# Kernel optimization log

Measured on AMD Instinct MI355X. Metric: run time of the kernel, lower is better.

Reference implementation:

```python
import jax, jax.numpy as jnp
import numpy as np

D_MODEL = 1024
N_HEADS = 16
HEAD_DIM = D_MODEL // N_HEADS
D_LATENT = 256
LAMBDA_DECAY = 0.01
TIME_STEP = 0.01  # get_timestamps spacing; wall-clock base cancels in diffs
CLAMP = 1e4


def setup_inputs() -> dict:
    key = jax.random.key(0)
    ks = jax.random.split(key, 8)
    B, S = 2, 2048
    def w(k, i, o):
        return jax.random.normal(k, (i, o), dtype=jnp.float32) * 0.02
    return {
        "x": jax.random.normal(ks[0], (B, S, D_MODEL), dtype=jnp.float32),
        "Wq": w(ks[1], D_MODEL, D_MODEL),
        "Wk": w(ks[2], D_MODEL, D_MODEL),
        "Wv": w(ks[3], D_MODEL, D_MODEL),
        "Wo": w(ks[4], D_MODEL, D_MODEL),
        "W_down_kv": w(ks[5], D_MODEL, D_LATENT),
        "W_up_k": w(ks[6], D_LATENT, D_MODEL),
        "W_up_v": w(ks[7], D_LATENT, D_MODEL),
    }


def reference(x, Wq, Wk, Wv, Wo, W_down_kv, W_up_k, W_up_v):
    B, S, _ = x.shape
    q = x @ Wq
    k = x @ Wk
    v = x @ Wv
    latent_kv = (k + v) @ W_down_kv            # [B,S,d_latent]
    k_rec = latent_kv @ W_up_k                 # [B,S,d_model]
    v_rec = latent_kv @ W_up_v
    # split heads -> [B,H,S,hd]
    def heads(t):
        return t.reshape(B, S, N_HEADS, HEAD_DIM).transpose(0, 2, 1, 3)
    qh, kh, vh = heads(q), heads(k_rec), heads(v_rec)
    scale = 1.0 / (jnp.sqrt(jnp.float32(D_MODEL)) + 1e-8)
    scores = jnp.einsum("bhqd,bhkd->bhqk", qh, kh) * scale
    scores = jnp.clip(jnp.nan_to_num(scores, nan=-1e9), -CLAMP, CLAMP)
    # time decay: |t_i - t_j| = TIME_STEP * |i - j| (wall-clock base cancels)
    idx = jnp.arange(S, dtype=jnp.float32)
    decay = jnp.exp(-LAMBDA_DECAY * TIME_STEP * jnp.abs(idx[:, None] - idx[None, :]))
    scores = scores * decay[None, None, :, :]
    scores = jnp.clip(jnp.nan_to_num(scores, nan=-1e9), -CLAMP, CLAMP)
    attn = jax.nn.softmax(scores, axis=-1)
    out = jnp.einsum("bhqk,bhkd->bhqd", attn, vh)
    out = out.transpose(0, 2, 1, 3).reshape(B, S, D_MODEL)
    return out @ Wo, latent_kv
```

## Files before the change

kernel.cpp:

```cpp
#include <hip/hip_runtime.h>
#include <hip/hip_bf16.h>
#include <cstdint>
#include <cstddef>

typedef __bf16 bf16;
typedef __bf16 bf16x8 __attribute__((ext_vector_type(8)));
typedef float f32x4 __attribute__((ext_vector_type(4)));

#define NB 2
#define SEQ 2048
#define DM 1024
#define MTOK 4096
#define DL 256
#define NH 16
#define HD 64

#define LOG2E 1.4426950408889634f

__device__ __forceinline__ void gload16(const void* g, void* l) {
  __builtin_amdgcn_global_load_lds((const __attribute__((address_space(1))) void*)g,
                                   (__attribute__((address_space(3))) void*)l, 16, 0, 0);
}
__device__ __forceinline__ float fast_exp2(float x) {
#if __has_builtin(__builtin_amdgcn_exp2f)
  return __builtin_amdgcn_exp2f(x);
#else
  float r; asm("v_exp_f32 %0, %1" : "=v"(r) : "v"(x)); return r;
#endif
}
__device__ __forceinline__ int xcd_swz(int orig, int nwg) {
  int x = orig & 7;
  int q = nwg >> 3, r = nwg & 7;
  int base = (x < r) ? x * (q + 1) : r * (q + 1) + (x - r) * q;
  return base + (orig >> 3);
}

__device__ __forceinline__ void transpose_dev(const float* __restrict__ in0,
                                              bf16* __restrict__ out, int R, int C,
                                              int c0, int r0, int tid, float (*tile)[33]) {
  int tx = tid & 31, ty = tid >> 5;
#pragma unroll
  for (int i = 0; i < 4; ++i) {
    int r = r0 + ty + 8 * i;
    tile[ty + 8 * i][tx] = in0[(size_t)r * C + c0 + tx];
  }
  __syncthreads();
  int c = tid >> 3, s = tid & 7;
  bf16 o4[4] __attribute__((aligned(8)));
#pragma unroll
  for (int j = 0; j < 4; ++j) o4[j] = (bf16)tile[4 * s + j][c];
  *reinterpret_cast<uint2*>(out + (size_t)(c0 + c) * R + r0 + 4 * s) =
      *reinterpret_cast<const uint2*>(o4);
}

__device__ __forceinline__ void cvt8_dev(const float* __restrict__ in, bf16* __restrict__ out,
                                         int blk, int tid) {
  int i = (blk * 256 + tid) * 8;
  float4 a = *reinterpret_cast<const float4*>(in + i);
  float4 b = *reinterpret_cast<const float4*>(in + i + 4);
  bf16 o[8] __attribute__((aligned(16)));
  o[0] = (bf16)a.x; o[1] = (bf16)a.y; o[2] = (bf16)a.z; o[3] = (bf16)a.w;
  o[4] = (bf16)b.x; o[5] = (bf16)b.y; o[6] = (bf16)b.z; o[7] = (bf16)b.w;
  *reinterpret_cast<uint4*>(out + i) = *reinterpret_cast<const uint4*>(o);
}

__device__ __forceinline__ void sum8_dev(const float* __restrict__ in0, const float* __restrict__ in1,
                                         bf16* __restrict__ out, int blk, int tid) {
  int i = (blk * 256 + tid) * 8;
  float4 a0 = *reinterpret_cast<const float4*>(in0 + i);
  float4 b0 = *reinterpret_cast<const float4*>(in0 + i + 4);
  float4 a1 = *reinterpret_cast<const float4*>(in1 + i);
  float4 b1 = *reinterpret_cast<const float4*>(in1 + i + 4);
  bf16 o[8] __attribute__((aligned(16)));
  o[0] = (bf16)(a0.x + a1.x); o[1] = (bf16)(a0.y + a1.y);
  o[2] = (bf16)(a0.z + a1.z); o[3] = (bf16)(a0.w + a1.w);
  o[4] = (bf16)(b0.x + b1.x); o[5] = (bf16)(b0.y + b1.y);
  o[6] = (bf16)(b0.z + b1.z); o[7] = (bf16)(b0.w + b1.w);
  *reinterpret_cast<uint4*>(out + i) = *reinterpret_cast<const uint4*>(o);
}

__global__ __launch_bounds__(256) void prep_kernel(const float* __restrict__ x,
                                                   const float* __restrict__ Wq,
                                                   const float* __restrict__ Wk,
                                                   const float* __restrict__ Wv,
                                                   const float* __restrict__ Wo,
                                                   const float* __restrict__ Wdn,
                                                   const float* __restrict__ Wuk,
                                                   const float* __restrict__ Wuv,
                                                   bf16* xbf, bf16* WqT, bf16* WoT, bf16* WdnT,
                                                   bf16* WukT, bf16* WuvT, bf16* Wkv) {
  __shared__ float tile[32][33];
  int id = blockIdx.x, tid = threadIdx.x;
  if (id < 2048) { cvt8_dev(x, xbf, id, tid); return; }
  id -= 2048;
  if (id < 512) { sum8_dev(Wk, Wv, Wkv, id, tid); return; }
  id -= 512;
  if (id < 1024) { transpose_dev(Wq, WqT, 1024, 1024, (id & 31) * 32, (id >> 5) * 32, tid, tile); return; }
  id -= 1024;
  if (id < 1024) { transpose_dev(Wo, WoT, 1024, 1024, (id & 31) * 32, (id >> 5) * 32, tid, tile); return; }
  id -= 1024;
  if (id < 256) { transpose_dev(Wdn, WdnT, 1024, 256, (id & 7) * 32, (id >> 3) * 32, tid, tile); return; }
  id -= 256;
  if (id < 256) { transpose_dev(Wuk, WukT, 256, 1024, (id & 31) * 32, (id >> 5) * 32, tid, tile); return; }
  id -= 256;
  transpose_dev(Wuv, WuvT, 256, 1024, (id & 31) * 32, (id >> 5) * 32, tid, tile);
}

template <int TN, int EPI>
__device__ __forceinline__ void gemm_core(const bf16* __restrict__ A, const bf16* __restrict__ Bt,
                                          bf16* __restrict__ O1, float* __restrict__ Of,
                                          int K, int bx, int by, bf16* As, bf16* Bs) {
  const int tid = threadIdx.x;
  const int lane = tid & 63;
  const int wv = tid >> 6;
  const int wr = wv >> 1, wc = wv & 1;
  const int row0 = bx * 128, col0 = by * TN;
  const int l15 = lane & 15;
  const int kq = (lane >> 4) * 8;
  constexpr int NR = TN / 32;
  constexpr int BSZ = TN * 32;

  const bf16* aS = A + (size_t)(row0 + (tid >> 2)) * K + (tid & 3) * 8;
  const bf16* bS = Bt + (size_t)(col0 + (tid >> 2)) * K + (tid & 3) * 8;
  const int d0 = tid * 8, d1 = tid * 8 + 2048;

  gload16(aS, As + d0); gload16(aS + (size_t)64 * K, As + d1);
  gload16(bS, Bs + d0);
  if constexpr (TN == 128) gload16(bS + (size_t)64 * K, Bs + d1);
  aS += 32; bS += 32;

  f32x4 acc[4][NR] = {};
  int cur = 0;
  for (int k0 = 0; k0 < K; k0 += 32) {
    __syncthreads();
    if (k0 + 32 < K) {
      const int nxA = (cur ^ 1) * 4096, nxB = (cur ^ 1) * BSZ;
      gload16(aS, As + nxA + d0); gload16(aS + (size_t)64 * K, As + nxA + d1);
      gload16(bS, Bs + nxB + d0);
      if constexpr (TN == 128) gload16(bS + (size_t)64 * K, Bs + nxB + d1);
      aS += 32; bS += 32;
    }
    const bf16* Ab = As + cur * 4096;
    const bf16* Bb = Bs + cur * BSZ;
    bf16x8 af[4], bfr[NR];
#pragma unroll
    for (int m = 0; m < 4; ++m)
      af[m] = *reinterpret_cast<const bf16x8*>(&Ab[(wr * 64 + m * 16 + l15) * 32 + kq]);
#pragma unroll
    for (int n = 0; n < NR; ++n)
      bfr[n] = *reinterpret_cast<const bf16x8*>(&Bb[(wc * (TN / 2) + n * 16 + l15) * 32 + kq]);
    __builtin_amdgcn_s_setprio(1);
#pragma unroll
    for (int m = 0; m < 4; ++m)
#pragma unroll
      for (int n = 0; n < NR; ++n)
        acc[m][n] = __builtin_amdgcn_mfma_f32_16x16x32_bf16(af[m], bfr[n], acc[m][n], 0, 0, 0);
    __builtin_amdgcn_s_setprio(0);
    cur ^= 1;
  }

  const int rbase = row0 + wr * 64 + (lane >> 4) * 4;
  const int cbase = col0 + wc * (TN / 2) + l15;
#pragma unroll
  for (int m = 0; m < 4; ++m) {
#pragma unroll
    for (int n = 0; n < NR; ++n) {
      const int cc = cbase + n * 16;
      if constexpr (EPI == 0) {
#pragma unroll
        for (int r = 0; r < 4; ++r)
          O1[(size_t)(rbase + m * 16 + r) * DM + cc] = (bf16)acc[m][n][r];
      } else if constexpr (EPI == 3) {
#pragma unroll
        for (int r = 0; r < 4; ++r)
          Of[(size_t)(rbase + m * 16 + r) * DM + cc] = acc[m][n][r];
      } else {
#pragma unroll
        for (int r = 0; r < 4; ++r)
          O1[(size_t)(rbase + m * 16 + r) * MTOK + cc] = (bf16)acc[m][n][r];
      }
    }
  }
}

__device__ __forceinline__ void gemm64_lat(const bf16* __restrict__ A, const bf16* __restrict__ Bt,
                                           bf16* __restrict__ O1, float* __restrict__ Of,
                                           int K, int bx, int by, bf16* As, bf16* Bs) {
  const int tid = threadIdx.x;
  const int lane = tid & 63;
  const int wv = tid >> 6;
  const int wr = wv >> 1, wc = wv & 1;
  const int row0 = bx * 64, col0 = by * 64;
  const int l15 = lane & 15;
  const int kq = (lane >> 4) * 8;

  const bf16* aS = A + (size_t)(row0 + (tid >> 2)) * K + (tid & 3) * 8;
  const bf16* bS = Bt + (size_t)(col0 + (tid >> 2)) * K + (tid & 3) * 8;
  const int d0 = tid * 8;

  gload16(aS, As + d0); gload16(bS, Bs + d0);
  aS += 32; bS += 32;

  f32x4 acc[2][2] = {};
  int cur = 0;
  for (int k0 = 0; k0 < K; k0 += 32) {
    __syncthreads();
    if (k0 + 32 < K) {
      const int nx = (cur ^ 1) * 2048;
      gload16(aS, As + nx + d0); gload16(bS, Bs + nx + d0);
      aS += 32; bS += 32;
    }
    const bf16* Ab = As + cur * 2048;
    const bf16* Bb = Bs + cur * 2048;
    bf16x8 af[2], bfr[2];
#pragma unroll
    for (int m = 0; m < 2; ++m)
      af[m] = *reinterpret_cast<const bf16x8*>(&Ab[(wr * 32 + m * 16 + l15) * 32 + kq]);
#pragma unroll
    for (int n = 0; n < 2; ++n)
      bfr[n] = *reinterpret_cast<const bf16x8*>(&Bb[(wc * 32 + n * 16 + l15) * 32 + kq]);
    __builtin_amdgcn_s_setprio(1);
#pragma unroll
    for (int m = 0; m < 2; ++m)
#pragma unroll
      for (int n = 0; n < 2; ++n)
        acc[m][n] = __builtin_amdgcn_mfma_f32_16x16x32_bf16(af[m], bfr[n], acc[m][n], 0, 0, 0);
    __builtin_amdgcn_s_setprio(0);
    cur ^= 1;
  }

  const int rbase = row0 + wr * 32 + (lane >> 4) * 4;
  const int cbase = col0 + wc * 32 + l15;
#pragma unroll
  for (int m = 0; m < 2; ++m)
#pragma unroll
    for (int n = 0; n < 2; ++n)
#pragma unroll
      for (int r = 0; r < 4; ++r) {
        float v = acc[m][n][r];
        O1[(size_t)(rbase + m * 16 + r) * DL + (cbase + n * 16)] = (bf16)v;
        Of[(size_t)(rbase + m * 16 + r) * DL + (cbase + n * 16)] = v;
      }
}

__global__ __launch_bounds__(256) void gemm_q_w(const bf16* __restrict__ xbf,
                                                const bf16* __restrict__ WqT, bf16* qbf,
                                                const bf16* __restrict__ WdnT,
                                                const bf16* __restrict__ Wkv, bf16* WkvdT) {
  __shared__ __align__(16) bf16 As[2 * 4096];
  __shared__ __align__(16) bf16 Bs[2 * 64 * 32];
  int id = xcd_swz(blockIdx.x, 544);
  if (id < 32)
    gemm_core<64, 0>(WdnT, Wkv, WkvdT, nullptr, DM, id >> 4, id & 15, As, Bs);
  else {
    int j = id - 32;
    gemm_core<64, 0>(xbf, WqT, qbf, nullptr, DM, j >> 4, j & 15, As, Bs);
  }
}

__global__ __launch_bounds__(256) void gemm_latent(const bf16* __restrict__ xbf,
                                                   const bf16* __restrict__ WkvdT,
                                                   bf16* latbf, float* out_lat) {
  __shared__ __align__(16) bf16 As[2 * 2048];
  __shared__ __align__(16) bf16 Bs[2 * 2048];
  int id = xcd_swz(blockIdx.x, 256);
  gemm64_lat(xbf, WkvdT, latbf, out_lat, DM, id >> 2, id & 3, As, Bs);
}

__global__ __launch_bounds__(256) void gemm_up(const bf16* __restrict__ latbf,
                                               const bf16* __restrict__ WukT,
                                               const bf16* __restrict__ WuvT,
                                               bf16* kbuf, bf16* vT) {
  __shared__ __align__(16) bf16 As[2 * 4096];
  __shared__ __align__(16) bf16 Bs[2 * 64 * 32];
  int id = xcd_swz(blockIdx.x, 1024);
  if (id < 512)
    gemm_core<64, 0>(latbf, WukT, kbuf, nullptr, DL, id >> 4, id & 15, As, Bs);
  else {
    int j = id - 512;
    gemm_core<64, 7>(WuvT, latbf, vT, nullptr, DL, j >> 6, j & 63, As, Bs);
  }
}

__global__ __launch_bounds__(256) void gemm_out(const bf16* __restrict__ ctx,
                                                const bf16* __restrict__ WoT, float* out0) {
  __shared__ __align__(16) bf16 As[2 * 4096];
  __shared__ __align__(16) bf16 Bs[2 * 64 * 32];
  int id = xcd_swz(blockIdx.x, 512);
  gemm_core<64, 3>(ctx, WoT, nullptr, out0, DM, id >> 4, id & 15, As, Bs);
}

__global__ __launch_bounds__(512) void attn_kernel(const bf16* __restrict__ Q,
                                                   const bf16* __restrict__ Kr,
                                                   const bf16* __restrict__ Vt,
                                                   bf16* __restrict__ Ctx) {
  __shared__ __align__(16) bf16 Ks[2 * 4096];
  __shared__ __align__(16) bf16 Vs[2 * 4096];
  __shared__ __align__(16) bf16 Ps[8192];
  const int work = xcd_swz(blockIdx.x, SEQ / 128 * NH * NB);
  const int qt = work & 15, h = (work >> 4) & 15, b = work >> 8;
  const int tid = threadIdx.x, lane = tid & 63, wv = tid >> 6;
  const int l15 = lane & 15, lg = lane >> 4;
  const int qbase = qt * 128 + wv * 16;
  const size_t tok0 = (size_t)b * SEQ;

  bf16x8 qf[2];
  {
    const bf16* qp = Q + (tok0 + qbase + l15) * DM + h * HD + lg * 8;
    qf[0] = *reinterpret_cast<const bf16x8*>(qp);
    qf[1] = *reinterpret_cast<const bf16x8*>(qp + 32);
  }

  const int r0s = tid >> 3;
  const int cc0 = (tid & 7) ^ (r0s & 7);
  const bf16* kS0 = Kr + (tok0 + r0s) * DM + h * HD + cc0 * 8;
  const bf16* vS0 = Vt + (size_t)(h * HD + r0s) * MTOK + tok0 + cc0 * 8;
  const int d0 = tid * 8;

  gload16(kS0, Ks + d0);
  gload16(vS0, Vs + d0);
  kS0 += 64 * DM; vS0 += 64;

  int koff[2][4], poffw[4], poffr[2];
  const int hsw = l15 & 7;
#pragma unroll
  for (int ks = 0; ks < 2; ++ks)
#pragma unroll
    for (int nf = 0; nf < 4; ++nf) {
      int row = nf * 16 + l15;
      koff[ks][nf] = row * 64 + (((ks * 4 + lg) ^ (row & 7)) * 8);
    }
  const int psBase = wv * 1024 + l15 * 64;
#pragma unroll
  for (int nf = 0; nf < 4; ++nf)
    poffw[nf] = psBase + (((nf * 2 + (lg >> 1)) ^ hsw) * 8) + (lg & 1) * 4;
#pragma unroll
  for (int ks = 0; ks < 2; ++ks)
    poffr[ks] = psBase + (((ks * 4 + lg) ^ hsw) * 8);

  bf16x8 ones;
#pragma unroll
  for (int j = 0; j < 8; ++j) ones[j] = (bf16)1.0f;

  f32x4 oacc[4] = {};
  f32x4 lacc = {};
  float dec[4][4];
  const float DEC2C = (1.0f / 32.0f) * LOG2E;
  const float NC2 = -1.0e-4f * LOG2E;
  const float E64 = 0.99362048f, IE64 = 1.00642051f;
  const int ib = -qbase - l15 + lg * 4;

  int cur = 0;
  for (int t = 0; t < SEQ / 64; ++t) {
    const int key0 = t * 64;
    __syncthreads();
    if (t + 1 < SEQ / 64) {
      const int nx = (cur ^ 1) * 4096;
      gload16(kS0, Ks + nx + d0);
      gload16(vS0, Vs + nx + d0);
      kS0 += 64 * DM; vS0 += 64;
    }
    {
      bool before = (key0 + 63 < qbase);
      bool afterp = (key0 >= qbase + 79);
      if (t == 0 || (!before && !afterp)) {
#pragma unroll
        for (int nf = 0; nf < 4; ++nf)
#pragma unroll
          for (int r = 0; r < 4; ++r) {
            float df = (float)(key0 + ib + nf * 16 + r);
            dec[nf][r] = DEC2C * fast_exp2(NC2 * fabsf(df));
          }
      } else {
        float mlt = before ? IE64 : E64;
#pragma unroll
        for (int nf = 0; nf < 4; ++nf)
#pragma unroll
          for (int r = 0; r < 4; ++r) dec[nf][r] *= mlt;
      }
    }
    const int kb = cur * 4096;

    f32x4 sc[4] = {};
    __builtin_amdgcn_s_setprio(1);
#pragma unroll
    for (int ks = 0; ks < 2; ++ks)
#pragma unroll
      for (int nf = 0; nf < 4; ++nf) {
        bf16x8 kf = *reinterpret_cast<const bf16x8*>(&Ks[kb + koff[ks][nf]]);
        sc[nf] = __builtin_amdgcn_mfma_f32_16x16x32_bf16(kf, qf[ks], sc[nf], 0, 0, 0);
      }
    __builtin_amdgcn_s_setprio(0);

#pragma unroll
    for (int nf = 0; nf < 4; ++nf) {
      bf16 t4[4] __attribute__((aligned(8)));
#pragma unroll
      for (int r = 0; r < 4; ++r) t4[r] = (bf16)fast_exp2(sc[nf][r] * dec[nf][r]);
      *reinterpret_cast<uint2*>(&Ps[poffw[nf]]) = *reinterpret_cast<const uint2*>(t4);
    }
    bf16x8 pb[2];
    pb[0] = *reinterpret_cast<const bf16x8*>(&Ps[poffr[0]]);
    pb[1] = *reinterpret_cast<const bf16x8*>(&Ps[poffr[1]]);

    __builtin_amdgcn_s_setprio(1);
#pragma unroll
    for (int ks = 0; ks < 2; ++ks) {
#pragma unroll
      for (int nf = 0; nf < 4; ++nf) {
        bf16x8 vf = *reinterpret_cast<const bf16x8*>(&Vs[kb + koff[ks][nf]]);
        oacc[nf] = __builtin_amdgcn_mfma_f32_16x16x32_bf16(vf, pb[ks], oacc[nf], 0, 0, 0);
      }
      lacc = __builtin_amdgcn_mfma_f32_16x16x32_bf16(ones, pb[ks], lacc, 0, 0, 0);
    }
    __builtin_amdgcn_s_setprio(0);
    cur ^= 1;
  }

  const float inv = 1.0f / lacc[0];
#pragma unroll
  for (int nf = 0; nf < 4; ++nf) {
    bf16 o4[4] __attribute__((aligned(8)));
#pragma unroll
    for (int r = 0; r < 4; ++r) o4[r] = (bf16)(oacc[nf][r] * inv);
    *reinterpret_cast<uint2*>(Ctx + (tok0 + qbase + l15) * DM + h * HD + nf * 16 + lg * 4) =
        *reinterpret_cast<const uint2*>(o4);
  }
}

extern "C" void kernel_launch(void* const* d_in, const int* in_sizes, int n_in,
                              void* d_out, int out_size, void* d_ws, size_t ws_size,
                              hipStream_t stream) {
  const float* x   = (const float*)d_in[0];
  const float* Wq  = (const float*)d_in[1];
  const float* Wk  = (const float*)d_in[2];
  const float* Wv  = (const float*)d_in[3];
  const float* Wo  = (const float*)d_in[4];
  const float* Wdn = (const float*)d_in[5];
  const float* Wuk = (const float*)d_in[6];
  const float* Wuv = (const float*)d_in[7];
  float* out0 = (float*)d_out;
  float* out_lat = out0 + (size_t)MTOK * DM;

  char* ws = (char*)d_ws;
  const size_t MB = 1u << 20;
  bf16* xbf   = (bf16*)(ws + 0);
  bf16* qbf   = (bf16*)(ws + 8 * MB);
  bf16* kbuf  = (bf16*)(ws + 16 * MB);
  bf16* Wkv   = kbuf;
  bf16* WkvdT = (bf16*)(ws + 18 * MB);
  bf16* vT    = (bf16*)(ws + 24 * MB);
  bf16* latbf = (bf16*)(ws + 32 * MB);
  bf16* WqT   = (bf16*)(ws + 34 * MB);
  bf16* WoT   = (bf16*)(ws + 36 * MB);
  bf16* WukT  = (bf16*)(ws + 38 * MB);
  bf16* WuvT  = (bf16*)(ws + 38 * MB + 512 * 1024);
  bf16* WdnT  = (bf16*)(ws + 39 * MB);
  bf16* ctx   = xbf;

  prep_kernel<<<5376, 256, 0, stream>>>(x, Wq, Wk, Wv, Wo, Wdn, Wuk, Wuv,
                                        xbf, WqT, WoT, WdnT, WukT, WuvT, Wkv);
  gemm_q_w<<<544, 256, 0, stream>>>(xbf, WqT, qbf, WdnT, Wkv, WkvdT);
  gemm_latent<<<256, 256, 0, stream>>>(xbf, WkvdT, latbf, out_lat);
  gemm_up<<<1024, 256, 0, stream>>>(latbf, WukT, WuvT, kbuf, vT);
  attn_kernel<<<512, 512, 0, stream>>>(qbf, kbuf, vT, ctx);
  gemm_out<<<512, 256, 0, stream>>>(ctx, WoT, out0);

  (void)in_sizes; (void)n_in; (void)out_size; (void)ws_size;
}
```

Before: 123.2 us.

## Double GEMM K-tile to 64 with XOR-swizzled LDS layout

```diff
diff --git a/kernel.cpp b/kernel.cpp
--- a/kernel.cpp
+++ b/kernel.cpp
@@ -106,7 +106,7 @@
   transpose_dev(Wuv, WuvT, 256, 1024, (id & 31) * 32, (id >> 5) * 32, tid, tile);
 }
 
-template <int TN, int EPI>
+template <int EPI>
 __device__ __forceinline__ void gemm_core(const bf16* __restrict__ A, const bf16* __restrict__ Bt,
                                           bf16* __restrict__ O1, float* __restrict__ Of,
                                           int K, int bx, int by, bf16* As, bf16* Bs) {
@@ -114,57 +114,81 @@
   const int lane = tid & 63;
   const int wv = tid >> 6;
   const int wr = wv >> 1, wc = wv & 1;
-  const int row0 = bx * 128, col0 = by * TN;
+  const int row0 = bx * 128, col0 = by * 64;
   const int l15 = lane & 15;
-  const int kq = (lane >> 4) * 8;
-  constexpr int NR = TN / 32;
-  constexpr int BSZ = TN * 32;
-
-  const bf16* aS = A + (size_t)(row0 + (tid >> 2)) * K + (tid & 3) * 8;
-  const bf16* bS = Bt + (size_t)(col0 + (tid >> 2)) * K + (tid & 3) * 8;
-  const int d0 = tid * 8, d1 = tid * 8 + 2048;
-
-  gload16(aS, As + d0); gload16(aS + (size_t)64 * K, As + d1);
-  gload16(bS, Bs + d0);
-  if constexpr (TN == 128) gload16(bS + (size_t)64 * K, Bs + d1);
-  aS += 32; bS += 32;
-
-  f32x4 acc[4][NR] = {};
+  const int lg = lane >> 4;
+
+  const int r0 = tid >> 3;
+  const int ccs = (tid & 7) ^ (r0 & 7);
+  const bf16* aS = A + (size_t)(row0 + r0) * K + ccs * 8;
+  const bf16* bS = Bt + (size_t)(col0 + r0) * K + ccs * 8;
+  const int dA = tid * 8;
+
+#pragma unroll
+  for (int i = 0; i < 4; ++i) gload16(aS + (size_t)(32 * i) * K, As + dA + 2048 * i);
+#pragma unroll
+  for (int j = 0; j < 2; ++j) gload16(bS + (size_t)(32 * j) * K, Bs + dA + 2048 * j);
+  aS += 64; bS += 64;
+
+  int aoff[4][2], boff[2][2];
+#pragma unroll
+  for (int m = 0; m < 4; ++m) {
+    int ra = wr * 64 + m * 16 + l15;
+#pragma unroll
+    for (int kk = 0; kk < 2; ++kk)
+      aoff[m][kk] = ra * 64 + (((kk * 4 + lg) ^ (ra & 7)) * 8);
+  }
+#pragma unroll
+  for (int n = 0; n < 2; ++n) {
+    int rb = wc * 32 + n * 16 + l15;
+#pragma unroll
+    for (int kk = 0; kk < 2; ++kk)
+      boff[n][kk] = rb * 64 + (((kk * 4 + lg) ^ (rb & 7)) * 8);
+  }
+
+  f32x4 acc[4][2] = {};
   int cur = 0;
-  for (int k0 = 0; k0 < K; k0 += 32) {
+  for (int k0 = 0; k0 < K; k0 += 64) {
     __syncthreads();
-    if (k0 + 32 < K) {
-      const int nxA = (cur ^ 1) * 4096, nxB = (cur ^ 1) * BSZ;
-      gload16(aS, As + nxA + d0); gload16(aS + (size_t)64 * K, As + nxA + d1);
-      gload16(bS, Bs + nxB + d0);
-      if constexpr (TN == 128) gload16(bS + (size_t)64 * K, Bs + nxB + d1);
-      aS += 32; bS += 32;
-    }
-    const bf16* Ab = As + cur * 4096;
-    const bf16* Bb = Bs + cur * BSZ;
-    bf16x8 af[4], bfr[NR];
+    if (k0 + 64 < K) {
+      const int nxA = (cur ^ 1) * 8192, nxB = (cur ^ 1) * 4096;
+#pragma unroll
+      for (int i = 0; i < 4; ++i) gload16(aS + (size_t)(32 * i) * K, As + nxA + dA + 2048 * i);
+#pragma unroll
+      for (int j = 0; j < 2; ++j) gload16(bS + (size_t)(32 * j) * K, Bs + nxB + dA + 2048 * j);
+      aS += 64; bS += 64;
+    }
+    const bf16* Ab = As + cur * 8192;
+    const bf16* Bb = Bs + cur * 4096;
+    bf16x8 af[4][2], bfr[2][2];
 #pragma unroll
     for (int m = 0; m < 4; ++m)
-      af[m] = *reinterpret_cast<const bf16x8*>(&Ab[(wr * 64 + m * 16 + l15) * 32 + kq]);
-#pragma unroll
-    for (int n = 0; n < NR; ++n)
-      bfr[n] = *reinterpret_cast<const bf16x8*>(&Bb[(wc * (TN / 2) + n * 16 + l15) * 32 + kq]);
+#pragma unroll
+      for (int kk = 0; kk < 2; ++kk)
+        af[m][kk] = *reinterpret_cast<const bf16x8*>(&Ab[aoff[m][kk]]);
+#pragma unroll
+    for (int n = 0; n < 2; ++n)
+#pragma unroll
+      for (int kk = 0; kk < 2; ++kk)
+        bfr[n][kk] = *reinterpret_cast<const bf16x8*>(&Bb[boff[n][kk]]);
     __builtin_amdgcn_s_setprio(1);
 #pragma unroll
-    for (int m = 0; m < 4; ++m)
-#pragma unroll
-      for (int n = 0; n < NR; ++n)
-        acc[m][n] = __builtin_amdgcn_mfma_f32_16x16x32_bf16(af[m], bfr[n], acc[m][n], 0, 0, 0);
+    for (int kk = 0; kk < 2; ++kk)
+#pragma unroll
+      for (int m = 0; m < 4; ++m)
+#pragma unroll
+        for (int n = 0; n < 2; ++n)
+          acc[m][n] = __builtin_amdgcn_mfma_f32_16x16x32_bf16(af[m][kk], bfr[n][kk], acc[m][n], 0, 0, 0);
     __builtin_amdgcn_s_setprio(0);
     cur ^= 1;
   }
 
   const int rbase = row0 + wr * 64 + (lane >> 4) * 4;
-  const int cbase = col0 + wc * (TN / 2) + l15;
+  const int cbase = col0 + wc * 32 + l15;
 #pragma unroll
   for (int m = 0; m < 4; ++m) {
 #pragma unroll
-    for (int n = 0; n < NR; ++n) {
+    for (int n = 0; n < 2; ++n) {
       const int cc = cbase + n * 16;
       if constexpr (EPI == 0) {
 #pragma unroll
@@ -192,39 +216,64 @@
   const int wr = wv >> 1, wc = wv & 1;
   const int row0 = bx * 64, col0 = by * 64;
   const int l15 = lane & 15;
-  const int kq = (lane >> 4) * 8;
-
-  const bf16* aS = A + (size_t)(row0 + (tid >> 2)) * K + (tid & 3) * 8;
-  const bf16* bS = Bt + (size_t)(col0 + (tid >> 2)) * K + (tid & 3) * 8;
-  const int d0 = tid * 8;
-
-  gload16(aS, As + d0); gload16(bS, Bs + d0);
-  aS += 32; bS += 32;
+  const int lg = lane >> 4;
+
+  const int r0 = tid >> 3;
+  const int ccs = (tid & 7) ^ (r0 & 7);
+  const bf16* aS = A + (size_t)(row0 + r0) * K + ccs * 8;
+  const bf16* bS = Bt + (size_t)(col0 + r0) * K + ccs * 8;
+  const int dA = tid * 8;
+
+#pragma unroll
+  for (int j = 0; j < 2; ++j) {
+    gload16(aS + (size_t)(32 * j) * K, As + dA + 2048 * j);
+    gload16(bS + (size_t)(32 * j) * K, Bs + dA + 2048 * j);
+  }
+  aS += 64; bS += 64;
+
+  int aoff[2][2], boff[2][2];
+#pragma unroll
+  for (int m = 0; m < 2; ++m) {
+    int ra = wr * 32 + m * 16 + l15;
+    int rb = wc * 32 + m * 16 + l15;
+#pragma unroll
+    for (int kk = 0; kk < 2; ++kk) {
+      aoff[m][kk] = ra * 64 + (((kk * 4 + lg) ^ (ra & 7)) * 8);
+      boff[m][kk] = rb * 64 + (((kk * 4 + lg) ^ (rb & 7)) * 8);
+    }
+  }
 
   f32x4 acc[2][2] = {};
   int cur = 0;
-  for (int k0 = 0; k0 < K; k0 += 32) {
+  for (int k0 = 0; k0 < K; k0 += 64) {
     __syncthreads();
-    if (k0 + 32 < K) {
-      const int nx = (cur ^ 1) * 2048;
-      gload16(aS, As + nx + d0); gload16(bS, Bs + nx + d0);
-      aS += 32; bS += 32;
-    }
-    const bf16* Ab = As + cur * 2048;
-    const bf16* Bb = Bs + cur * 2048;
-    bf16x8 af[2], bfr[2];
+    if (k0 + 64 < K) {
+      const int nx = (cur ^ 1) * 4096;
+#pragma unroll
+      for (int j = 0; j < 2; ++j) {
+        gload16(aS + (size_t)(32 * j) * K, As + nx + dA + 2048 * j);
+        gload16(bS + (size_t)(32 * j) * K, Bs + nx + dA + 2048 * j);
+      }
+      aS += 64; bS += 64;
+    }
+    const bf16* Ab = As + cur * 4096;
+    const bf16* Bb = Bs + cur * 4096;
+    bf16x8 af[2][2], bfr[2][2];
 #pragma unroll
     for (int m = 0; m < 2; ++m)
-      af[m] = *reinterpret_cast<const bf16x8*>(&Ab[(wr * 32 + m * 16 + l15) * 32 + kq]);
-#pragma unroll
-    for (int n = 0; n < 2; ++n)
-      bfr[n] = *reinterpret_cast<const bf16x8*>(&Bb[(wc * 32 + n * 16 + l15) * 32 + kq]);
+#pragma unroll
+      for (int kk = 0; kk < 2; ++kk) {
+        af[m][kk] = *reinterpret_cast<const bf16x8*>(&Ab[aoff[m][kk]]);
+        bfr[m][kk] = *reinterpret_cast<const bf16x8*>(&Bb[boff[m][kk]]);
+      }
     __builtin_amdgcn_s_setprio(1);
 #pragma unroll
-    for (int m = 0; m < 2; ++m)
-#pragma unroll
-      for (int n = 0; n < 2; ++n)
-        acc[m][n] = __builtin_amdgcn_mfma_f32_16x16x32_bf16(af[m], bfr[n], acc[m][n], 0, 0, 0);
+    for (int kk = 0; kk < 2; ++kk)
+#pragma unroll
+      for (int m = 0; m < 2; ++m)
+#pragma unroll
+        for (int n = 0; n < 2; ++n)
+          acc[m][n] = __builtin_amdgcn_mfma_f32_16x16x32_bf16(af[m][kk], bfr[n][kk], acc[m][n], 0, 0, 0);
     __builtin_amdgcn_s_setprio(0);
     cur ^= 1;
   }
@@ -247,22 +296,22 @@
                                                 const bf16* __restrict__ WqT, bf16* qbf,
                                                 const bf16* __restrict__ WdnT,
                                                 const bf16* __restrict__ Wkv, bf16* WkvdT) {
-  __shared__ __align__(16) bf16 As[2 * 4096];
-  __shared__ __align__(16) bf16 Bs[2 * 64 * 32];
+  __shared__ __align__(16) bf16 As[2 * 8192];
+  __shared__ __align__(16) bf16 Bs[2 * 4096];
   int id = xcd_swz(blockIdx.x, 544);
   if (id < 32)
-    gemm_core<64, 0>(WdnT, Wkv, WkvdT, nullptr, DM, id >> 4, id & 15, As, Bs);
+    gemm_core<0>(WdnT, Wkv, WkvdT, nullptr, DM, id >> 4, id & 15, As, Bs);
   else {
     int j = id - 32;
-    gemm_core<64, 0>(xbf, WqT, qbf, nullptr, DM, j >> 4, j & 15, As, Bs);
+    gemm_core<0>(xbf, WqT, qbf, nullptr, DM, j >> 4, j & 15, As, Bs);
   }
 }
 
 __global__ __launch_bounds__(256) void gemm_latent(const bf16* __restrict__ xbf,
                                                    const bf16* __restrict__ WkvdT,
                                                    bf16* latbf, float* out_lat) {
-  __shared__ __align__(16) bf16 As[2 * 2048];
-  __shared__ __align__(16) bf16 Bs[2 * 2048];
+  __shared__ __align__(16) bf16 As[2 * 4096];
+  __shared__ __align__(16) bf16 Bs[2 * 4096];
   int id = xcd_swz(blockIdx.x, 256);
   gemm64_lat(xbf, WkvdT, latbf, out_lat, DM, id >> 2, id & 3, As, Bs);
 }
@@ -271,23 +320,23 @@
                                                const bf16* __restrict__ WukT,
                                                const bf16* __restrict__ WuvT,
                                                bf16* kbuf, bf16* vT) {
-  __shared__ __align__(16) bf16 As[2 * 4096];
-  __shared__ __align__(16) bf16 Bs[2 * 64 * 32];
+  __shared__ __align__(16) bf16 As[2 * 8192];
+  __shared__ __align__(16) bf16 Bs[2 * 4096];
   int id = xcd_swz(blockIdx.x, 1024);
   if (id < 512)
-    gemm_core<64, 0>(latbf, WukT, kbuf, nullptr, DL, id >> 4, id & 15, As, Bs);
+    gemm_core<0>(latbf, WukT, kbuf, nullptr, DL, id >> 4, id & 15, As, Bs);
   else {
     int j = id - 512;
-    gemm_core<64, 7>(WuvT, latbf, vT, nullptr, DL, j >> 6, j & 63, As, Bs);
+    gemm_core<7>(WuvT, latbf, vT, nullptr, DL, j >> 6, j & 63, As, Bs);
   }
 }
 
 __global__ __launch_bounds__(256) void gemm_out(const bf16* __restrict__ ctx,
                                                 const bf16* __restrict__ WoT, float* out0) {
-  __shared__ __align__(16) bf16 As[2 * 4096];
-  __shared__ __align__(16) bf16 Bs[2 * 64 * 32];
+  __shared__ __align__(16) bf16 As[2 * 8192];
+  __shared__ __align__(16) bf16 Bs[2 * 4096];
   int id = xcd_swz(blockIdx.x, 512);
-  gemm_core<64, 3>(ctx, WoT, nullptr, out0, DM, id >> 4, id & 15, As, Bs);
+  gemm_core<3>(ctx, WoT, nullptr, out0, DM, id >> 4, id & 15, As, Bs);
 }
 
 __global__ __launch_bounds__(512) void attn_kernel(const bf16* __restrict__ Q,
```

Result: faster. 115.4 us (median of 2 runs) (-6.3%).
